# Kernel tuning notes

Hardware: AMD Instinct MI355X
Metric: run time of the kernel (lower is better)

## Reference

```python
import math
import jax, jax.numpy as jnp
import numpy as np

N_HEAD = 16
KNN = 4                     # config.knn_num
MEM_FRAC = 8.0              # config.mem_frac
INFLUENCE = 1.0             # config.knn_softmax_influence
RESID_FOUND = 0.5           # from set_resid_frac(resid_frac=0.5) (assumed split)
RESID_CURR = 0.5


def setup_inputs() -> dict:
    key = jax.random.key(0)
    ks = jax.random.split(key, 7)
    B, T, C, H, M = 1, 1024, 1024, N_HEAD, 8192
    d = C // H
    return {
        "x": jax.random.normal(ks[0], (B, T, C), jnp.float32),
        "c_attn_w": jax.random.normal(ks[1], (3 * C, C), jnp.float32) * 0.02,
        "c_attn_b": jax.random.normal(ks[2], (3 * C,), jnp.float32) * 0.01,
        "c_proj_w": jax.random.normal(ks[3], (C, C), jnp.float32) * 0.02,
        "c_proj_b": jax.random.normal(ks[4], (C,), jnp.float32) * 0.01,
        "key_store": jax.random.normal(ks[5], (H, M, d), jnp.float32),
        "value_store": jax.random.normal(ks[6], (H, M, d), jnp.float32),
    }


def _knn_get(att, k, q, v, key_store, value_store):
    # Faithful vectorized version of knn_get (batch must be 1, as in the
    # original whose scatter offsets i*t are only valid for b==1).
    B, H, T, d = k.shape
    scale = 1.0 / math.sqrt(d)
    # last-query attention row over all keys: (B,H,T)
    a = att[:, :, -1, :]
    # mem_frac thresholding (bookkeeping_frac falsy -> skipped)
    a = jnp.where(a < 1.0 / (MEM_FRAC * T), 0.0, a)
    sel = (a != 0.0)[0]                      # (H,T) selected positions
    kh, qh, vh = k[0], q[0], v[0]            # (H,T,d)
    # exact L2 search = faiss.IndexFlatL2: d2 = |k|^2 - 2 k.s + |s|^2
    d2 = (jnp.sum(kh * kh, -1, keepdims=True)
          - 2.0 * jnp.einsum('htd,hmd->htm', kh, key_store)
          + jnp.sum(key_store * key_store, -1)[:, None, :])   # (H,T,M)
    _, idx = jax.lax.top_k(-d2, KNN)         # (H,T,K) nearest neighbors
    idx = jnp.maximum(idx, 0)                # idx[idx<0]=0
    keys_f = jnp.take_along_axis(key_store[:, None, :, :], idx[..., None], axis=2)   # (H,T,K,d)
    vals_f = jnp.take_along_axis(value_store[:, None, :, :], idx[..., None], axis=2)
    # not resid_only: prepend current key/value -> stack size K+1
    keys_all = jnp.concatenate([kh[:, :, None, :], keys_f], axis=2)   # (H,T,S,d)
    vals_all = jnp.concatenate([vh[:, :, None, :], vals_f], axis=2)
    attf = jnp.einsum('htd,htsd->hts', qh, keys_all) * scale
    attf = jnp.where(jnp.isnan(attf), -jnp.inf, attf)
    w = jax.nn.softmax(attf * INFLUENCE, axis=-1)                     # softmax over the stack dim
    vals = jnp.einsum('hts,htsd->htd', w, vals_all)
    vals = vals * RESID_FOUND + vh * RESID_CURR                       # resid mix branch
    v_new = jnp.where(sel[..., None], vals, vh)                       # scatter back
    return v_new[None]                                                # (1,H,T,d)


def reference(x, c_attn_w, c_attn_b, c_proj_w, c_proj_b, key_store, value_store):
    B, T, C = x.shape
    H = key_store.shape[0]
    d = C // H
    qkv = x @ c_attn_w.T + c_attn_b
    q, k, v = jnp.split(qkv, 3, axis=2)
    heads = lambda t: t.reshape(B, T, H, d).transpose(0, 2, 1, 3)
    q, k, v = heads(q), heads(k), heads(v)
    logits = jnp.einsum('bhqd,bhkd->bhqk', q, k) * (1.0 / math.sqrt(d))
    causal = jnp.tril(jnp.ones((T, T), bool))
    logits = jnp.where(causal, logits, -jnp.inf)
    att = jax.nn.softmax(logits, axis=-1)
    # knn_get runs under torch.no_grad in the original
    v_new = jax.lax.stop_gradient(_knn_get(att, k, q, v, key_store, value_store))
    y = jnp.einsum('bhqk,bhkd->bhqd', att, v_new)   # dropout p=0 (eval)
    y = y.transpose(0, 2, 1, 3).reshape(B, T, C)
    return y @ c_proj_w.T + c_proj_b
```

## Files before the change

### kernel.cpp

```cpp
#include <hip/hip_runtime.h>
#include <math.h>

#define NH 16
#define TT 1024
#define CC 1024
#define DD 64
#define MM 8192
#define MQ 4
#define MQS (MM / MQ)

typedef __attribute__((ext_vector_type(8))) short short8;
typedef __attribute__((ext_vector_type(4))) float f32x4;

__device__ __forceinline__ float wredsum(float x) {
#pragma unroll
  for (int o = 32; o; o >>= 1) x += __shfl_xor(x, o);
  return x;
}
__device__ __forceinline__ unsigned int bf16rn(float x) {
  unsigned int u = __float_as_uint(x);
  return (u + 0x7fffu + ((u >> 16) & 1u)) >> 16;
}
__device__ __forceinline__ float bf16f(unsigned int h) {
  return __uint_as_float(h << 16);
}

__device__ __forceinline__ void ins4(float d, int i, float vd[4], int vi[4]) {
  if (d < vd[3] || (d == vd[3] && i < vi[3])) {
    vd[3] = d; vi[3] = i;
#pragma unroll
    for (int s = 3; s > 0; --s) {
      bool sw = (vd[s] < vd[s - 1]) || (vd[s] == vd[s - 1] && vi[s] < vi[s - 1]);
      if (sw) {
        float td = vd[s]; vd[s] = vd[s - 1]; vd[s - 1] = td;
        int ti = vi[s]; vi[s] = vi[s - 1]; vi[s - 1] = ti;
      }
    }
  }
}

__device__ __forceinline__ void stage_rows8_swz(const char* gRow0, size_t gStride, char* lds, int lane) {
  int rr = lane >> 3;
  int c = (lane & 7) ^ rr;
  __builtin_amdgcn_global_load_lds(
      (const __attribute__((address_space(1))) unsigned int*)(gRow0 + (size_t)rr * gStride + (c << 4)),
      (__attribute__((address_space(3))) unsigned int*)lds, 16, 0, 0);
}

__device__ __forceinline__ void conv_chunk(const float* __restrict__ src,
                                           char* __restrict__ hi, char* __restrict__ lo, int gc) {
  const float* p = src + ((size_t)gc << 3);
  float4 f0 = *(const float4*)p;
  float4 f1 = *(const float4*)(p + 4);
  float f[8] = {f0.x, f0.y, f0.z, f0.w, f1.x, f1.y, f1.z, f1.w};
  short8 hv, lv;
#pragma unroll
  for (int e = 0; e < 8; ++e) {
    unsigned hb = bf16rn(f[e]);
    hv[e] = (short)hb;
    lv[e] = (short)bf16rn(f[e] - bf16f(hb));
  }
  size_t off = (size_t)gc << 4;
  *(short8*)(hi + off) = hv;
  *(short8*)(lo + off) = lv;
}

__global__ void __launch_bounds__(256) convert_all(
    const float* __restrict__ x, char* __restrict__ xhi, char* __restrict__ xlo,
    const float* __restrict__ Wa, char* __restrict__ wahi, char* __restrict__ walo,
    const float* __restrict__ Wp, char* __restrict__ wphi, char* __restrict__ wplo,
    const float* __restrict__ ks, char* __restrict__ khi, char* __restrict__ klo,
    float* __restrict__ kn2)
{
  int b = blockIdx.x, tid = threadIdx.x;
  if (b < 512) { conv_chunk(x, xhi, xlo, b * 256 + tid); return; }
  if (b < 2048) { conv_chunk(Wa, wahi, walo, (b - 512) * 256 + tid); return; }
  if (b < 2560) { conv_chunk(Wp, wphi, wplo, (b - 2048) * 256 + tid); return; }
  int gc = (b - 2560) * 256 + tid;
  const float* p = ks + ((size_t)gc << 3);
  float4 f0 = *(const float4*)p;
  float4 f1 = *(const float4*)(p + 4);
  float f[8] = {f0.x, f0.y, f0.z, f0.w, f1.x, f1.y, f1.z, f1.w};
  float s = 0.f;
  short8 hv, lv;
#pragma unroll
  for (int e = 0; e < 8; ++e) {
    s = fmaf(f[e], f[e], s);
    unsigned hb = bf16rn(f[e]);
    hv[e] = (short)hb;
    lv[e] = (short)bf16rn(f[e] - bf16f(hb));
  }
  size_t off = (size_t)gc << 4;
  *(short8*)(khi + off) = hv;
  *(short8*)(klo + off) = lv;
  s += __shfl_xor(s, 1);
  s += __shfl_xor(s, 2);
  s += __shfl_xor(s, 4);
  if ((tid & 7) == 0) kn2[gc >> 3] = -0.5f * s;
}

__global__ void __launch_bounds__(256) gemm_qkv(
    const char* __restrict__ xhi, const char* __restrict__ xlo,
    const char* __restrict__ wahi, const char* __restrict__ walo,
    const float* __restrict__ ba, char* __restrict__ qhi, char* __restrict__ qlo)
{
  int n0 = blockIdx.x * 128, m0 = blockIdx.y * 64;
  int tid = threadIdx.x, lane = tid & 63, w = tid >> 6;
  int wr = w >> 1, wc = w & 1;
  int lr = lane & 15, lc = lane >> 4;
  __shared__ __align__(16) char smem[49152];
  char* sAhi = smem;
  char* sAlo = smem + 8192;
  char* sBhi = smem + 16384;
  char* sBlo = smem + 32768;
  f32x4 acc[2][4];
#pragma unroll
  for (int i = 0; i < 2; ++i)
#pragma unroll
    for (int j = 0; j < 4; ++j) acc[i][j] = (f32x4){0.f, 0.f, 0.f, 0.f};

  for (int kb = 0; kb < 16; ++kb) {
    if (kb) __syncthreads();
#pragma unroll
    for (int c8 = 0; c8 < 2; ++c8) {
      int r8 = w * 16 + c8 * 8;
      stage_rows8_swz(xhi + (size_t)(m0 + r8) * 2048 + (size_t)kb * 128, 2048, sAhi + r8 * 128, lane);
      stage_rows8_swz(xlo + (size_t)(m0 + r8) * 2048 + (size_t)kb * 128, 2048, sAlo + r8 * 128, lane);
    }
#pragma unroll
    for (int c8 = 0; c8 < 4; ++c8) {
      int r8 = w * 32 + c8 * 8;
      stage_rows8_swz(wahi + (size_t)(n0 + r8) * 2048 + (size_t)kb * 128, 2048, sBhi + r8 * 128, lane);
      stage_rows8_swz(walo + (size_t)(n0 + r8) * 2048 + (size_t)kb * 128, 2048, sBlo + r8 * 128, lane);
    }
    __syncthreads();
#pragma unroll
    for (int kh = 0; kh < 2; ++kh) {
      short8 ah[2], al[2], bh[4], bl[4];
#pragma unroll
      for (int mi = 0; mi < 2; ++mi) {
        int ra = wr * 32 + mi * 16 + lr;
        int ca = ((kh * 4 + lc) ^ (ra & 7)) << 4;
        ah[mi] = *(const short8*)(sAhi + ra * 128 + ca);
        al[mi] = *(const short8*)(sAlo + ra * 128 + ca);
      }
#pragma unroll
      for (int nj = 0; nj < 4; ++nj) {
        int rb = wc * 64 + nj * 16 + lr;
        int cb = ((kh * 4 + lc) ^ (rb & 7)) << 4;
        bh[nj] = *(const short8*)(sBhi + rb * 128 + cb);
        bl[nj] = *(const short8*)(sBlo + rb * 128 + cb);
      }
#pragma unroll
      for (int mi = 0; mi < 2; ++mi)
#pragma unroll
        for (int nj = 0; nj < 4; ++nj) {
          acc[mi][nj] = __builtin_amdgcn_mfma_f32_16x16x32_bf16(ah[mi], bh[nj], acc[mi][nj], 0, 0, 0);
          acc[mi][nj] = __builtin_amdgcn_mfma_f32_16x16x32_bf16(al[mi], bh[nj], acc[mi][nj], 0, 0, 0);
          acc[mi][nj] = __builtin_amdgcn_mfma_f32_16x16x32_bf16(ah[mi], bl[nj], acc[mi][nj], 0, 0, 0);
        }
    }
  }

  __syncthreads();
  char* hbuf = smem + w * 9216;
  char* lbuf = hbuf + 4608;
#pragma unroll
  for (int mi = 0; mi < 2; ++mi)
#pragma unroll
    for (int nj = 0; nj < 4; ++nj)
#pragma unroll
      for (int r = 0; r < 4; ++r) {
        int row = mi * 16 + lc * 4 + r;
        int col = nj * 16 + lr;
        float v = acc[mi][nj][r] + ba[n0 + wc * 64 + col];
        unsigned hb = bf16rn(v);
        *(unsigned short*)(hbuf + row * 144 + col * 2) = (unsigned short)hb;
        *(unsigned short*)(lbuf + row * 144 + col * 2) = (unsigned short)bf16rn(v - bf16f(hb));
      }
#pragma unroll
  for (int ps = 0; ps < 4; ++ps) {
    int rr = ps * 8 + (lane >> 3);
    int c = lane & 7;
    size_t gb = ((size_t)(m0 + wr * 32 + rr) * 3072 + n0 + wc * 64) * 2 + (c << 4);
    *(uint4*)(qhi + gb) = *(const uint4*)(hbuf + rr * 144 + c * 16);
    *(uint4*)(qlo + gb) = *(const uint4*)(lbuf + rr * 144 + c * 16);
  }
}

#define QSLDS 2304
__global__ void __launch_bounds__(512) qk_softmax(
    const char* __restrict__ qhi, const char* __restrict__ qlo,
    char* __restrict__ attB, float* __restrict__ attlast)
{
  int rb = blockIdx.x, h = blockIdx.y;
  int i0 = rb * 32;
  int tid = threadIdx.x, lane = tid & 63, w = tid >> 6;
  int wr = w >> 2, wcg = w & 3;
  int lr = lane & 15, lc = lane >> 4;
  __shared__ float redm[2][16][4];
  __shared__ float reds[2][16][4];
  __shared__ __align__(16) char tb[8][2 * QSLDS];

  int iq = i0 + wr * 16 + lr;
  short8 ah[2], al[2];
  {
    size_t qb = (size_t)iq * 6144 + h * 128;
#pragma unroll
    for (int kh = 0; kh < 2; ++kh) {
      size_t off = qb + ((kh * 4 + lc) << 4);
      ah[kh] = *(const short8*)(qhi + off);
      al[kh] = *(const short8*)(qlo + off);
    }
  }

  f32x4 acc[16];
#pragma unroll
  for (int nt = 0; nt < 16; ++nt) acc[nt] = (f32x4){0.f, 0.f, 0.f, 0.f};

  int maxj = i0 + 31;
#pragma unroll
  for (int nt = 0; nt < 16; ++nt) {
    if (wcg * 256 + nt * 16 <= maxj) {
      int jr = wcg * 256 + nt * 16 + lr;
      size_t kb = (size_t)jr * 6144 + 2048 + h * 128;
      short8 bh[2], bl[2];
#pragma unroll
      for (int kh = 0; kh < 2; ++kh) {
        size_t off = kb + ((kh * 4 + lc) << 4);
        bh[kh] = *(const short8*)(qhi + off);
        bl[kh] = *(const short8*)(qlo + off);
      }
#pragma unroll
      for (int kh = 0; kh < 2; ++kh) {
        acc[nt] = __builtin_amdgcn_mfma_f32_16x16x32_bf16(ah[kh], bh[kh], acc[nt], 0, 0, 0);
        acc[nt] = __builtin_amdgcn_mfma_f32_16x16x32_bf16(al[kh], bh[kh], acc[nt], 0, 0, 0);
        acc[nt] = __builtin_amdgcn_mfma_f32_16x16x32_bf16(ah[kh], bl[kh], acc[nt], 0, 0, 0);
      }
    }
  }

  int iv[4];
  float pmax[4];
#pragma unroll
  for (int r = 0; r < 4; ++r) {
    iv[r] = i0 + wr * 16 + lc * 4 + r;
    pmax[r] = -INFINITY;
  }
#pragma unroll
  for (int nt = 0; nt < 16; ++nt) {
    int j = wcg * 256 + nt * 16 + lr;
#pragma unroll
    for (int r = 0; r < 4; ++r) {
      float v = (j <= iv[r]) ? acc[nt][r] * 0.125f : -INFINITY;
      acc[nt][r] = v;
      pmax[r] = fmaxf(pmax[r], v);
    }
  }
#pragma unroll
  for (int o = 1; o <= 8; o <<= 1)
#pragma unroll
    for (int r = 0; r < 4; ++r) pmax[r] = fmaxf(pmax[r], __shfl_xor(pmax[r], o));
  if (lr == 0) {
#pragma unroll
    for (int r = 0; r < 4; ++r) redm[wr][lc * 4 + r][wcg] = pmax[r];
  }
  __syncthreads();
  float rowm[4];
#pragma unroll
  for (int r = 0; r < 4; ++r) {
    float* q = redm[wr][lc * 4 + r];
    rowm[r] = fmaxf(fmaxf(q[0], q[1]), fmaxf(q[2], q[3]));
  }

  float psum[4] = {0.f, 0.f, 0.f, 0.f};
#pragma unroll
  for (int nt = 0; nt < 16; ++nt)
#pragma unroll
    for (int r = 0; r < 4; ++r) {
      float e = __expf(acc[nt][r] - rowm[r]);
      acc[nt][r] = e;
      psum[r] += e;
    }
#pragma unroll
  for (int o = 1; o <= 8; o <<= 1)
#pragma unroll
    for (int r = 0; r < 4; ++r) psum[r] += __shfl_xor(psum[r], o);
  if (lr == 0) {
#pragma unroll
    for (int r = 0; r < 4; ++r) reds[wr][lc * 4 + r][wcg] = psum[r];
  }
  __syncthreads();
  float inv[4];
#pragma unroll
  for (int r = 0; r < 4; ++r) {
    float* q = reds[wr][lc * 4 + r];
    inv[r] = 1.0f / (q[0] + q[1] + q[2] + q[3]);
  }

  char* mybuf = tb[w];
  int iv0 = i0 + wr * 16;
#pragma unroll
  for (int cc = 0; cc < 4; ++cc) {
#pragma unroll
    for (int q = 0; q < 4; ++q) {
      int nt = cc * 4 + q;
      int col = q * 16 + lr;
#pragma unroll
      for (int r = 0; r < 4; ++r) {
        int row = lc * 4 + r;
        float v = acc[nt][r] * inv[r];
        unsigned hb = bf16rn(v);
        unsigned lb = bf16rn(v - bf16f(hb));
        *(unsigned short*)(mybuf + row * 144 + col * 2) = (unsigned short)hb;
        *(unsigned short*)(mybuf + QSLDS + row * 144 + col * 2) = (unsigned short)lb;
        if (iv[r] == 1023) attlast[(h << 10) + wcg * 256 + cc * 64 + col] = v;
      }
    }
    __syncthreads();
#pragma unroll
    for (int half = 0; half < 2; ++half) {
      int rr = (lane >> 3) + half * 8;
      int c = lane & 7;
      int rowg = iv0 + rr;
      uint4 hv = *(const uint4*)(mybuf + rr * 144 + c * 16);
      uint4 lv = *(const uint4*)(mybuf + QSLDS + rr * 144 + c * 16);
      size_t basep = ((size_t)h << 22) + ((size_t)rowg << 12)
                   + (size_t)(((wcg << 2) + cc) << 7) + (size_t)(c << 4);
      *(uint4*)(attB + basep) = hv;
      *(uint4*)(attB + basep + 2048) = lv;
    }
    __syncthreads();
  }
}

#define BUFB 16384

#define TOPK_STEP(PAR, DO_STAGE)                                              \
  {                                                                           \
    if (DO_STAGE) {                                                           \
      _Pragma("unroll")                                                       \
      for (int i2 = 0; i2 < 4; ++i2) {                                        \
        __builtin_amdgcn_global_load_lds(                                     \
            (const __attribute__((address_space(1))) unsigned int*)stsrc[i2], \
            (__attribute__((address_space(3))) unsigned int*)(stdst[i2] + ((PAR) ^ 16384)), \
            16, 0, 0);                                                        \
        stsrc[i2] += 8192;                                                    \
      }                                                                       \
    }                                                                         \
    f32x4 acc[4];                                                             \
    _Pragma("unroll")                                                         \
    for (int ms = 0; ms < 4; ++ms)                                            \
      acc[ms] = *(const f32x4*)(knp + ms * 64);                               \
    knp += 256;                                                               \
    _Pragma("unroll")                                                         \
    for (int ms = 0; ms < 4; ++ms) {                                          \
      short8 ah0 = *(const short8*)(frg[ms * 2 + 0] + (PAR));                 \
      short8 al0 = *(const short8*)(frg[ms * 2 + 0] + (PAR) + 8192);          \
      short8 ah1 = *(const short8*)(frg[ms * 2 + 1] + (PAR));                 \
      short8 al1 = *(const short8*)(frg[ms * 2 + 1] + (PAR) + 8192);          \
      acc[ms] = __builtin_amdgcn_mfma_f32_16x16x32_bf16(ah0, bhi[0], acc[ms], 0, 0, 0); \
      acc[ms] = __builtin_amdgcn_mfma_f32_16x16x32_bf16(al0, bhi[0], acc[ms], 0, 0, 0); \
      acc[ms] = __builtin_amdgcn_mfma_f32_16x16x32_bf16(ah0, blo[0], acc[ms], 0, 0, 0); \
      acc[ms] = __builtin_amdgcn_mfma_f32_16x16x32_bf16(ah1, bhi[1], acc[ms], 0, 0, 0); \
      acc[ms] = __builtin_amdgcn_mfma_f32_16x16x32_bf16(al1, bhi[1], acc[ms], 0, 0, 0); \
      acc[ms] = __builtin_amdgcn_mfma_f32_16x16x32_bf16(ah1, blo[1], acc[ms], 0, 0, 0); \
    }                                                                         \
    float pk[16];                                                             \
    _Pragma("unroll")                                                         \
    for (int ms = 0; ms < 4; ++ms)                                            \
      _Pragma("unroll")                                                       \
      for (int r = 0; r < 4; ++r) {                                           \
        unsigned u = __float_as_uint(acc[ms][r]);                             \
        pk[ms * 4 + r] = __uint_as_float((u & ~15u) | (unsigned)(ms * 4 + r)); \
      }                                                                       \
    float mx = pk[0];                                                         \
    _Pragma("unroll")                                                         \
    for (int c = 1; c < 16; ++c) mx = fmaxf(mx, pk[c]);                       \
    while (mx > ba[3]) {                                                      \
      unsigned pb = __float_as_uint(mx);                                      \
      int cl = pb & 15;                                                       \
      ba[3] = mx; bi_[3] = mg0 + ((cl & 12) << 2) + (cl & 3);                 \
      _Pragma("unroll")                                                       \
      for (int s = 3; s > 0; --s)                                             \
        if (ba[s] > ba[s - 1]) {                                              \
          float td = ba[s]; ba[s] = ba[s - 1]; ba[s - 1] = td;                \
          int ti = bi_[s]; bi_[s] = bi_[s - 1]; bi_[s - 1] = ti;              \
        }                                                                     \
      _Pragma("unroll")                                                       \
      for (int c2 = 0; c2 < 16; ++c2)                                         \
        if (pk[c2] == mx) pk[c2] = -3.0e38f;                                  \
      mx = pk[0];                                                             \
      _Pragma("unroll")                                                       \
      for (int c2 = 1; c2 < 16; ++c2) mx = fmaxf(mx, pk[c2]);                 \
    }                                                                         \
    mg0 += 64;                                                                \
    __syncthreads();                                                          \
  }

__global__ void __launch_bounds__(256, 4) topk_mfma(
    const char* __restrict__ qhi, const char* __restrict__ qlo,
    const char* __restrict__ khi, const char* __restrict__ klo,
    const float* __restrict__ kn2, float* __restrict__ pd, int* __restrict__ pi)
{
  int bid = blockIdx.x;
  int h = bid & 15, ttile = (bid >> 4) & 15, mq = bid >> 8;
  int tid = threadIdx.x, lane = tid & 63, w = tid >> 6;
  int t0 = ttile * 64 + w * 16;
  __shared__ __align__(16) char smem[2 * BUFB];

  short8 bhi[2], blo[2];
  {
    int t = t0 + (lane & 15);
    size_t rb = (size_t)t * 6144 + 2048 + h * 128;
#pragma unroll
    for (int kh = 0; kh < 2; ++kh) {
      size_t off = rb + ((kh * 4 + (lane >> 4)) << 4);
      bhi[kh] = *(const short8*)(qhi + off);
      blo[kh] = *(const short8*)(qlo + off);
    }
  }

  const char* ghi = khi + ((size_t)h * MM + (size_t)mq * MQS) * 128;
  const char* glo = klo + ((size_t)h * MM + (size_t)mq * MQS) * 128;
  const char* knp = (const char*)(kn2 + (size_t)h * MM + (size_t)mq * MQS + ((lane >> 4) << 2));

  float ba[4] = {-3.0e38f, -3.0e38f, -3.0e38f, -3.0e38f};
  int   bi_[4] = {-1, -1, -1, -1};

  const char* stsrc[4];
  char* stdst[4];
  {
    int rr = lane >> 3;
    size_t laneoff = (size_t)rr * 128 + (((lane & 7) ^ rr) << 4);
#pragma unroll
    for (int i2 = 0; i2 < 4; ++i2) {
      int s = w * 4 + i2;
      stsrc[i2] = ((s < 8) ? (ghi + s * 1024) : (glo + (s - 8) * 1024)) + laneoff;
      stdst[i2] = smem + s * 1024;
    }
  }
  char* frg[8];
#pragma unroll
  for (int ms = 0; ms < 4; ++ms)
#pragma unroll
    for (int kh = 0; kh < 2; ++kh) {
      int mloc = ms * 16 + (lane & 15);
      int c = kh * 4 + (lane >> 4);
      frg[ms * 2 + kh] = smem + mloc * 128 + ((c ^ (mloc & 7)) << 4);
    }

#pragma unroll
  for (int i2 = 0; i2 < 4; ++i2) {
    __builtin_amdgcn_global_load_lds(
        (const __attribute__((address_space(1))) unsigned int*)stsrc[i2],
        (__attribute__((address_space(3))) unsigned int*)stdst[i2], 16, 0, 0);
    stsrc[i2] += 8192;
  }
  __syncthreads();

  int mg0 = mq * MQS + ((lane >> 4) << 2);
  for (int it2 = 0; it2 < 16; ++it2) {
    TOPK_STEP(0, true)
    TOPK_STEP(16384, (it2 < 15))
  }

  float bd[4];
#pragma unroll
  for (int s = 0; s < 4; ++s) bd[s] = ba[s] * -2.0f;
#pragma unroll
  for (int st = 16; st <= 32; st <<= 1) {
    float sd[4]; int si[4];
#pragma unroll
    for (int s = 0; s < 4; ++s) {
      sd[s] = __shfl_xor(bd[s], st);
      si[s] = __shfl_xor(bi_[s], st);
    }
#pragma unroll
    for (int s = 0; s < 4; ++s) ins4(sd[s], si[s], bd, bi_);
  }
  if (lane < 16) {
    size_t o = (((size_t)mq * NH + h) * TT + (t0 + lane)) * 4;
#pragma unroll
    for (int s = 0; s < 4; ++s) { pd[o + s] = bd[s]; pi[o + s] = bi_[s]; }
  }
}

__global__ void __launch_bounds__(1024) knn_attend(
    const char* __restrict__ qhi, const char* __restrict__ qlo,
    const float* __restrict__ attlast,
    const float* __restrict__ pd, const int* __restrict__ pi,
    const float* __restrict__ kstore, const float* __restrict__ vstore,
    char* __restrict__ vThi, char* __restrict__ vTlo)
{
  __shared__ __align__(16) unsigned short hiT[64][72];
  __shared__ __align__(16) unsigned short loT[64][72];
  int tid = threadIdx.x, lane = tid & 63, w = tid >> 6;
  int h = blockIdx.x >> 4, t0 = (blockIdx.x & 15) << 6;

#pragma unroll
  for (int i = 0; i < 4; ++i) {
    int t = t0 + w * 4 + i;
    int g = (h << 10) + t;

    float fd[4]; int fi[4];
    {
      size_t o = ((size_t)(lane & 3) * (NH * TT) + g) * 4;
#pragma unroll
      for (int s = 0; s < 4; ++s) { fd[s] = pd[o + s]; fi[s] = pi[o + s]; }
#pragma unroll
      for (int st = 1; st <= 2; st <<= 1) {
        float sd[4]; int si[4];
#pragma unroll
        for (int s = 0; s < 4; ++s) {
          sd[s] = __shfl_xor(fd[s], st);
          si[s] = __shfl_xor(fi[s], st);
        }
#pragma unroll
        for (int s = 0; s < 4; ++s) ins4(sd[s], si[s], fd, fi);
      }
    }

    size_t rb = (size_t)t * 6144 + h * 128 + lane * 2;
    float q = bf16f(*(const unsigned short*)(qhi + rb)) + bf16f(*(const unsigned short*)(qlo + rb));
    float k = bf16f(*(const unsigned short*)(qhi + rb + 2048)) + bf16f(*(const unsigned short*)(qlo + rb + 2048));
    float v = bf16f(*(const unsigned short*)(qhi + rb + 4096)) + bf16f(*(const unsigned short*)(qlo + rb + 4096));
    float al = attlast[g];
    bool sel = al >= (1.0f / 8192.0f);

    float attf[5], vf[5];
    attf[0] = wredsum(q * k) * 0.125f;
    vf[0] = v;
#pragma unroll
    for (int s = 1; s < 5; ++s) {
      int m = fi[s - 1];
      const float* kp = kstore + ((size_t)h * MM + m) * DD;
      const float* vp = vstore + ((size_t)h * MM + m) * DD;
      attf[s] = wredsum(q * kp[lane]) * 0.125f;
      vf[s] = vp[lane];
    }
    float mx = attf[0];
#pragma unroll
    for (int s = 1; s < 5; ++s) mx = fmaxf(mx, attf[s]);
    float wgt[5], sum = 0.f;
#pragma unroll
    for (int s = 0; s < 5; ++s) { wgt[s] = __expf(attf[s] - mx); sum += wgt[s]; }
    float inv = 1.0f / sum;
    float vals = 0.f;
#pragma unroll
    for (int s = 0; s < 5; ++s) vals = fmaf(wgt[s] * inv, vf[s], vals);
    float r = 0.5f * vals + 0.5f * v;
    float vn = sel ? r : v;

    unsigned hb = bf16rn(vn);
    hiT[lane][t - t0] = (unsigned short)hb;
    loT[lane][t - t0] = (unsigned short)bf16rn(vn - bf16f(hb));
  }
  __syncthreads();

  int half = tid >> 9;
  int idx = tid & 511;
  int r = idx >> 3, c = idx & 7;
  const unsigned short* src = half ? &loT[r][c * 8] : &hiT[r][c * 8];
  uint4 vv = *(const uint4*)src;
  char* dst = (half ? vTlo : vThi) + (size_t)((h << 6) + r) * 2048 + ((size_t)t0 << 1) + (c << 4);
  *(uint4*)dst = vv;
}

__global__ void __launch_bounds__(256) gemm_attv(
    const char* __restrict__ attB, const char* __restrict__ vThi, const char* __restrict__ vTlo,
    char* __restrict__ Yhi, char* __restrict__ Ylo)
{
  int h = blockIdx.y, m0 = blockIdx.x * 128;
  const char* aBase = attB + (size_t)h * 4194304;
  int tid = threadIdx.x, lane = tid & 63, w = tid >> 6;
  int wr = w >> 1, wc = w & 1;
  __shared__ __align__(16) char smem[49152];
  char* sAhi = smem;
  char* sAlo = smem + 16384;
  char* sBhi = smem + 32768;
  char* sBlo = smem + 40960;
  f32x4 acc[4][2];
#pragma unroll
  for (int i = 0; i < 4; ++i)
#pragma unroll
    for (int j = 0; j < 2; ++j) acc[i][j] = (f32x4){0.f, 0.f, 0.f, 0.f};
  int lr = lane & 15, lc = lane >> 4;
  int kbEnd = ((m0 + 127) >> 6) + 1;
  if (kbEnd > 16) kbEnd = 16;
  for (int kb = 0; kb < kbEnd; ++kb) {
    if (kb) __syncthreads();
#pragma unroll
    for (int c8 = 0; c8 < 4; ++c8) {
      int r8 = w * 32 + c8 * 8;
      stage_rows8_swz(aBase + (size_t)(m0 + r8) * 4096 + (size_t)kb * 128, 4096, sAhi + r8 * 128, lane);
      stage_rows8_swz(aBase + (size_t)(m0 + r8) * 4096 + 2048 + (size_t)kb * 128, 4096, sAlo + r8 * 128, lane);
    }
#pragma unroll
    for (int c8 = 0; c8 < 2; ++c8) {
      int r8 = w * 16 + c8 * 8;
      stage_rows8_swz(vThi + (size_t)((h << 6) + r8) * 2048 + (size_t)kb * 128, 2048, sBhi + r8 * 128, lane);
      stage_rows8_swz(vTlo + (size_t)((h << 6) + r8) * 2048 + (size_t)kb * 128, 2048, sBlo + r8 * 128, lane);
    }
    __syncthreads();
#pragma unroll
    for (int kh = 0; kh < 2; ++kh) {
      short8 ah[4], al[4], bh[2], bl[2];
#pragma unroll
      for (int f = 0; f < 4; ++f) {
        int ra = wr * 64 + f * 16 + lr;
        int ca = ((kh * 4 + lc) ^ (ra & 7)) << 4;
        ah[f] = *(const short8*)(sAhi + ra * 128 + ca);
        al[f] = *(const short8*)(sAlo + ra * 128 + ca);
      }
#pragma unroll
      for (int f = 0; f < 2; ++f) {
        int rbr = wc * 32 + f * 16 + lr;
        int cb = ((kh * 4 + lc) ^ (rbr & 7)) << 4;
        bh[f] = *(const short8*)(sBhi + rbr * 128 + cb);
        bl[f] = *(const short8*)(sBlo + rbr * 128 + cb);
      }
#pragma unroll
      for (int mi = 0; mi < 4; ++mi)
#pragma unroll
        for (int nj = 0; nj < 2; ++nj) {
          acc[mi][nj] = __builtin_amdgcn_mfma_f32_16x16x32_bf16(ah[mi], bh[nj], acc[mi][nj], 0, 0, 0);
          acc[mi][nj] = __builtin_amdgcn_mfma_f32_16x16x32_bf16(al[mi], bh[nj], acc[mi][nj], 0, 0, 0);
          acc[mi][nj] = __builtin_amdgcn_mfma_f32_16x16x32_bf16(ah[mi], bl[nj], acc[mi][nj], 0, 0, 0);
        }
    }
  }
#pragma unroll
  for (int mi = 0; mi < 4; ++mi)
#pragma unroll
    for (int nj = 0; nj < 2; ++nj)
#pragma unroll
      for (int r = 0; r < 4; ++r) {
        int m = m0 + wr * 64 + mi * 16 + lc * 4 + r;
        int n = (h << 6) + wc * 32 + nj * 16 + lr;
        float v = acc[mi][nj][r];
        unsigned hb = bf16rn(v);
        size_t off = ((size_t)m * 1024 + n) * 2;
        *(unsigned short*)(Yhi + off) = (unsigned short)hb;
        *(unsigned short*)(Ylo + off) = (unsigned short)bf16rn(v - bf16f(hb));
      }
}

__global__ void __launch_bounds__(256) gemm_out(
    const char* __restrict__ yhi, const char* __restrict__ ylo,
    const char* __restrict__ wphi, const char* __restrict__ wplo,
    const float* __restrict__ bp, float* __restrict__ out)
{
  int n0 = blockIdx.x * 64, m0 = blockIdx.y * 64;
  int tid = threadIdx.x, lane = tid & 63, w = tid >> 6;
  int wr = w >> 1, wc = w & 1;
  int lr = lane & 15, lc = lane >> 4;
  __shared__ __align__(16) char smem[32768];
  char* sAhi = smem;
  char* sAlo = smem + 8192;
  char* sBhi = smem + 16384;
  char* sBlo = smem + 24576;
  f32x4 acc[2][2];
#pragma unroll
  for (int i = 0; i < 2; ++i)
#pragma unroll
    for (int j = 0; j < 2; ++j) acc[i][j] = (f32x4){0.f, 0.f, 0.f, 0.f};

  for (int kb = 0; kb < 16; ++kb) {
    if (kb) __syncthreads();
#pragma unroll
    for (int c8 = 0; c8 < 2; ++c8) {
      int r8 = w * 16 + c8 * 8;
      stage_rows8_swz(yhi + (size_t)(m0 + r8) * 2048 + (size_t)kb * 128, 2048, sAhi + r8 * 128, lane);
      stage_rows8_swz(ylo + (size_t)(m0 + r8) * 2048 + (size_t)kb * 128, 2048, sAlo + r8 * 128, lane);
      stage_rows8_swz(wphi + (size_t)(n0 + r8) * 2048 + (size_t)kb * 128, 2048, sBhi + r8 * 128, lane);
      stage_rows8_swz(wplo + (size_t)(n0 + r8) * 2048 + (size_t)kb * 128, 2048, sBlo + r8 * 128, lane);
    }
    __syncthreads();
#pragma unroll
    for (int kh = 0; kh < 2; ++kh) {
      short8 ah[2], al[2], bh[2], bl[2];
#pragma unroll
      for (int mi = 0; mi < 2; ++mi) {
        int ra = wr * 32 + mi * 16 + lr;
        int ca = ((kh * 4 + lc) ^ (ra & 7)) << 4;
        ah[mi] = *(const short8*)(sAhi + ra * 128 + ca);
        al[mi] = *(const short8*)(sAlo + ra * 128 + ca);
      }
#pragma unroll
      for (int nj = 0; nj < 2; ++nj) {
        int rb = wc * 32 + nj * 16 + lr;
        int cb = ((kh * 4 + lc) ^ (rb & 7)) << 4;
        bh[nj] = *(const short8*)(sBhi + rb * 128 + cb);
        bl[nj] = *(const short8*)(sBlo + rb * 128 + cb);
      }
#pragma unroll
      for (int mi = 0; mi < 2; ++mi)
#pragma unroll
        for (int nj = 0; nj < 2; ++nj) {
          acc[mi][nj] = __builtin_amdgcn_mfma_f32_16x16x32_bf16(ah[mi], bh[nj], acc[mi][nj], 0, 0, 0);
          acc[mi][nj] = __builtin_amdgcn_mfma_f32_16x16x32_bf16(al[mi], bh[nj], acc[mi][nj], 0, 0, 0);
          acc[mi][nj] = __builtin_amdgcn_mfma_f32_16x16x32_bf16(ah[mi], bl[nj], acc[mi][nj], 0, 0, 0);
        }
    }
  }
#pragma unroll
  for (int mi = 0; mi < 2; ++mi)
#pragma unroll
    for (int nj = 0; nj < 2; ++nj)
#pragma unroll
      for (int r = 0; r < 4; ++r) {
        int m = m0 + wr * 32 + mi * 16 + lc * 4 + r;
        int n = n0 + wc * 32 + nj * 16 + lr;
        out[(size_t)m * 1024 + n] = acc[mi][nj][r] + bp[n];
      }
}

extern "C" void kernel_launch(void* const* d_in, const int* in_sizes, int n_in,
                              void* d_out, int out_size, void* d_ws, size_t ws_size,
                              hipStream_t stream) {
  (void)in_sizes; (void)n_in; (void)out_size; (void)ws_size;
  const float* x  = (const float*)d_in[0];
  const float* Wa = (const float*)d_in[1];
  const float* ba = (const float*)d_in[2];
  const float* Wp = (const float*)d_in[3];
  const float* bp = (const float*)d_in[4];
  const float* Ks = (const float*)d_in[5];
  const float* Vs = (const float*)d_in[6];
  float* out = (float*)d_out;

  char* base = (char*)d_ws;
  char* xhi  = base;
  char* xlo  = base + 0x200000;
  char* wahi = base + 0x400000;
  char* walo = base + 0xA00000;
  char* khi  = base + 0x1000000;
  char* klo  = base + 0x2000000;
  char*  attB = base;
  char* tail = base + 0x4000000;
  char* qhi = tail;
  char* qlo = tail + 0x600000;
  float* attlast = (float*)(tail + 0xC00000);
  float* kn2     = (float*)(tail + 0xC10000);
  float* pd      = (float*)(tail + 0xC90000);
  int*   pi      = (int*)(tail + 0xE90000);
  char* vThi = tail + 0x1090000;
  char* vTlo = tail + 0x1290000;
  char* yhi  = tail + 0x1490000;
  char* ylo  = tail + 0x1690000;
  char* wphi = tail + 0x1890000;
  char* wplo = tail + 0x1A90000;

  hipLaunchKernelGGL(convert_all, dim3(6656), dim3(256), 0, stream,
                     x, xhi, xlo, Wa, wahi, walo, Wp, wphi, wplo, Ks, khi, klo, kn2);
  hipLaunchKernelGGL(gemm_qkv, dim3(24, 16), dim3(256), 0, stream,
                     (const char*)xhi, (const char*)xlo, (const char*)wahi, (const char*)walo,
                     ba, qhi, qlo);
  hipLaunchKernelGGL(topk_mfma, dim3(16 * 16 * MQ), dim3(256), 0, stream,
                     (const char*)qhi, (const char*)qlo, (const char*)khi, (const char*)klo,
                     kn2, pd, pi);
  hipLaunchKernelGGL(qk_softmax, dim3(32, 16), dim3(512), 0, stream,
                     (const char*)qhi, (const char*)qlo, attB, attlast);
  hipLaunchKernelGGL(knn_attend, dim3(256), dim3(1024), 0, stream,
                     (const char*)qhi, (const char*)qlo, attlast, pd, pi, Ks, Vs, vThi, vTlo);
  hipLaunchKernelGGL(gemm_attv, dim3(8, 16), dim3(256), 0, stream,
                     (const char*)attB, (const char*)vThi, (const char*)vTlo, yhi, ylo);
  hipLaunchKernelGGL(gemm_out, dim3(16, 16), dim3(256), 0, stream,
                     (const char*)yhi, (const char*)ylo, (const char*)wphi, (const char*)wplo,
                     bp, out);
}
```

Baseline: 217.0 us.

## Fuse QK softmax with PV product, compute last attention row separately

```diff
diff --git a/kernel.cpp b/kernel.cpp
--- a/kernel.cpp
+++ b/kernel.cpp
@@ -188,150 +188,47 @@
   }
 }
 
-#define QSLDS 2304
-__global__ void __launch_bounds__(512) qk_softmax(
-    const char* __restrict__ qhi, const char* __restrict__ qlo,
-    char* __restrict__ attB, float* __restrict__ attlast)
+__global__ void __launch_bounds__(1024) attlast_k(
+    const char* __restrict__ qhi, const char* __restrict__ qlo, float* __restrict__ attlast)
 {
-  int rb = blockIdx.x, h = blockIdx.y;
-  int i0 = rb * 32;
-  int tid = threadIdx.x, lane = tid & 63, w = tid >> 6;
-  int wr = w >> 2, wcg = w & 3;
-  int lr = lane & 15, lc = lane >> 4;
-  __shared__ float redm[2][16][4];
-  __shared__ float reds[2][16][4];
-  __shared__ __align__(16) char tb[8][2 * QSLDS];
-
-  int iq = i0 + wr * 16 + lr;
-  short8 ah[2], al[2];
-  {
-    size_t qb = (size_t)iq * 6144 + h * 128;
-#pragma unroll
-    for (int kh = 0; kh < 2; ++kh) {
-      size_t off = qb + ((kh * 4 + lc) << 4);
-      ah[kh] = *(const short8*)(qhi + off);
-      al[kh] = *(const short8*)(qlo + off);
-    }
-  }
-
-  f32x4 acc[16];
-#pragma unroll
-  for (int nt = 0; nt < 16; ++nt) acc[nt] = (f32x4){0.f, 0.f, 0.f, 0.f};
-
-  int maxj = i0 + 31;
-#pragma unroll
-  for (int nt = 0; nt < 16; ++nt) {
-    if (wcg * 256 + nt * 16 <= maxj) {
-      int jr = wcg * 256 + nt * 16 + lr;
-      size_t kb = (size_t)jr * 6144 + 2048 + h * 128;
-      short8 bh[2], bl[2];
-#pragma unroll
-      for (int kh = 0; kh < 2; ++kh) {
-        size_t off = kb + ((kh * 4 + lc) << 4);
-        bh[kh] = *(const short8*)(qhi + off);
-        bl[kh] = *(const short8*)(qlo + off);
-      }
-#pragma unroll
-      for (int kh = 0; kh < 2; ++kh) {
-        acc[nt] = __builtin_amdgcn_mfma_f32_16x16x32_bf16(ah[kh], bh[kh], acc[nt], 0, 0, 0);
-        acc[nt] = __builtin_amdgcn_mfma_f32_16x16x32_bf16(al[kh], bh[kh], acc[nt], 0, 0, 0);
-        acc[nt] = __builtin_amdgcn_mfma_f32_16x16x32_bf16(ah[kh], bl[kh], acc[nt], 0, 0, 0);
-      }
-    }
-  }
-
-  int iv[4];
-  float pmax[4];
-#pragma unroll
-  for (int r = 0; r < 4; ++r) {
-    iv[r] = i0 + wr * 16 + lc * 4 + r;
-    pmax[r] = -INFINITY;
-  }
-#pragma unroll
-  for (int nt = 0; nt < 16; ++nt) {
-    int j = wcg * 256 + nt * 16 + lr;
-#pragma unroll
-    for (int r = 0; r < 4; ++r) {
-      float v = (j <= iv[r]) ? acc[nt][r] * 0.125f : -INFINITY;
-      acc[nt][r] = v;
-      pmax[r] = fmaxf(pmax[r], v);
-    }
-  }
-#pragma unroll
-  for (int o = 1; o <= 8; o <<= 1)
-#pragma unroll
-    for (int r = 0; r < 4; ++r) pmax[r] = fmaxf(pmax[r], __shfl_xor(pmax[r], o));
-  if (lr == 0) {
-#pragma unroll
-    for (int r = 0; r < 4; ++r) redm[wr][lc * 4 + r][wcg] = pmax[r];
-  }
-  __syncthreads();
-  float rowm[4];
-#pragma unroll
-  for (int r = 0; r < 4; ++r) {
-    float* q = redm[wr][lc * 4 + r];
-    rowm[r] = fmaxf(fmaxf(q[0], q[1]), fmaxf(q[2], q[3]));
-  }
-
-  float psum[4] = {0.f, 0.f, 0.f, 0.f};
-#pragma unroll
-  for (int nt = 0; nt < 16; ++nt)
-#pragma unroll
-    for (int r = 0; r < 4; ++r) {
-      float e = __expf(acc[nt][r] - rowm[r]);
-      acc[nt][r] = e;
-      psum[r] += e;
-    }
-#pragma unroll
-  for (int o = 1; o <= 8; o <<= 1)
-#pragma unroll
-    for (int r = 0; r < 4; ++r) psum[r] += __shfl_xor(psum[r], o);
-  if (lr == 0) {
-#pragma unroll
-    for (int r = 0; r < 4; ++r) reds[wr][lc * 4 + r][wcg] = psum[r];
-  }
-  __syncthreads();
-  float inv[4];
-#pragma unroll
-  for (int r = 0; r < 4; ++r) {
-    float* q = reds[wr][lc * 4 + r];
-    inv[r] = 1.0f / (q[0] + q[1] + q[2] + q[3]);
-  }
-
-  char* mybuf = tb[w];
-  int iv0 = i0 + wr * 16;
-#pragma unroll
-  for (int cc = 0; cc < 4; ++cc) {
-#pragma unroll
-    for (int q = 0; q < 4; ++q) {
-      int nt = cc * 4 + q;
-      int col = q * 16 + lr;
-#pragma unroll
-      for (int r = 0; r < 4; ++r) {
-        int row = lc * 4 + r;
-        float v = acc[nt][r] * inv[r];
-        unsigned hb = bf16rn(v);
-        unsigned lb = bf16rn(v - bf16f(hb));
-        *(unsigned short*)(mybuf + row * 144 + col * 2) = (unsigned short)hb;
-        *(unsigned short*)(mybuf + QSLDS + row * 144 + col * 2) = (unsigned short)lb;
-        if (iv[r] == 1023) attlast[(h << 10) + wcg * 256 + cc * 64 + col] = v;
-      }
-    }
-    __syncthreads();
-#pragma unroll
-    for (int half = 0; half < 2; ++half) {
-      int rr = (lane >> 3) + half * 8;
-      int c = lane & 7;
-      int rowg = iv0 + rr;
-      uint4 hv = *(const uint4*)(mybuf + rr * 144 + c * 16);
-      uint4 lv = *(const uint4*)(mybuf + QSLDS + rr * 144 + c * 16);
-      size_t basep = ((size_t)h << 22) + ((size_t)rowg << 12)
-                   + (size_t)(((wcg << 2) + cc) << 7) + (size_t)(c << 4);
-      *(uint4*)(attB + basep) = hv;
-      *(uint4*)(attB + basep + 2048) = lv;
-    }
-    __syncthreads();
-  }
+  int h = blockIdx.x;
+  int j = threadIdx.x, lane = j & 63, wv = j >> 6;
+  __shared__ float qrow[64];
+  __shared__ float redmx[16], redsm[16];
+  if (j < 64) {
+    size_t qb = (size_t)1023 * 6144 + h * 128 + j * 2;
+    qrow[j] = bf16f(*(const unsigned short*)(qhi + qb)) + bf16f(*(const unsigned short*)(qlo + qb));
+  }
+  __syncthreads();
+  size_t kb = (size_t)j * 6144 + 2048 + (size_t)h * 128;
+  float s = 0.f;
+#pragma unroll
+  for (int c8 = 0; c8 < 8; ++c8) {
+    short8 khv = *(const short8*)(qhi + kb + c8 * 16);
+    short8 klv = *(const short8*)(qlo + kb + c8 * 16);
+#pragma unroll
+    for (int e = 0; e < 8; ++e) {
+      float kv = bf16f((unsigned short)khv[e]) + bf16f((unsigned short)klv[e]);
+      s = fmaf(kv, qrow[c8 * 8 + e], s);
+    }
+  }
+  s *= 0.125f;
+  float m = s;
+#pragma unroll
+  for (int o = 32; o; o >>= 1) m = fmaxf(m, __shfl_xor(m, o));
+  if (lane == 0) redmx[wv] = m;
+  __syncthreads();
+  float M = redmx[0];
+#pragma unroll
+  for (int q = 1; q < 16; ++q) M = fmaxf(M, redmx[q]);
+  float e = __expf(s - M);
+  float ws = wredsum(e);
+  if (lane == 0) redsm[wv] = ws;
+  __syncthreads();
+  float S = redsm[0];
+#pragma unroll
+  for (int q = 1; q < 16; ++q) S += redsm[q];
+  attlast[(h << 10) + j] = e / S;
 }
 
 #define BUFB 16384
@@ -567,83 +464,189 @@
   *(uint4*)dst = vv;
 }
 
-__global__ void __launch_bounds__(256) gemm_attv(
-    const char* __restrict__ attB, const char* __restrict__ vThi, const char* __restrict__ vTlo,
+#define QSLDS 2304
+__global__ void __launch_bounds__(512) qk_softmax_pv(
+    const char* __restrict__ qhi, const char* __restrict__ qlo,
+    const char* __restrict__ vThi, const char* __restrict__ vTlo,
     char* __restrict__ Yhi, char* __restrict__ Ylo)
 {
-  int h = blockIdx.y, m0 = blockIdx.x * 128;
-  const char* aBase = attB + (size_t)h * 4194304;
+  int rb = blockIdx.x, h = blockIdx.y;
+  int i0 = rb * 32;
   int tid = threadIdx.x, lane = tid & 63, w = tid >> 6;
-  int wr = w >> 1, wc = w & 1;
-  __shared__ __align__(16) char smem[49152];
-  char* sAhi = smem;
-  char* sAlo = smem + 16384;
-  char* sBhi = smem + 32768;
-  char* sBlo = smem + 40960;
-  f32x4 acc[4][2];
-#pragma unroll
-  for (int i = 0; i < 4; ++i)
-#pragma unroll
-    for (int j = 0; j < 2; ++j) acc[i][j] = (f32x4){0.f, 0.f, 0.f, 0.f};
+  int wr = w >> 2, wcg = w & 3;
   int lr = lane & 15, lc = lane >> 4;
-  int kbEnd = ((m0 + 127) >> 6) + 1;
-  if (kbEnd > 16) kbEnd = 16;
-  for (int kb = 0; kb < kbEnd; ++kb) {
-    if (kb) __syncthreads();
-#pragma unroll
-    for (int c8 = 0; c8 < 4; ++c8) {
-      int r8 = w * 32 + c8 * 8;
-      stage_rows8_swz(aBase + (size_t)(m0 + r8) * 4096 + (size_t)kb * 128, 4096, sAhi + r8 * 128, lane);
-      stage_rows8_swz(aBase + (size_t)(m0 + r8) * 4096 + 2048 + (size_t)kb * 128, 4096, sAlo + r8 * 128, lane);
-    }
-#pragma unroll
-    for (int c8 = 0; c8 < 2; ++c8) {
-      int r8 = w * 16 + c8 * 8;
-      stage_rows8_swz(vThi + (size_t)((h << 6) + r8) * 2048 + (size_t)kb * 128, 2048, sBhi + r8 * 128, lane);
-      stage_rows8_swz(vTlo + (size_t)((h << 6) + r8) * 2048 + (size_t)kb * 128, 2048, sBlo + r8 * 128, lane);
-    }
-    __syncthreads();
+  __shared__ float redm[2][16][4];
+  __shared__ float reds[2][16][4];
+  __shared__ __align__(16) char tb[8][2 * QSLDS];
+
+  int iq = i0 + wr * 16 + lr;
+  short8 ah[2], al[2];
+  {
+    size_t qb = (size_t)iq * 6144 + h * 128;
 #pragma unroll
     for (int kh = 0; kh < 2; ++kh) {
-      short8 ah[4], al[4], bh[2], bl[2];
-#pragma unroll
-      for (int f = 0; f < 4; ++f) {
-        int ra = wr * 64 + f * 16 + lr;
-        int ca = ((kh * 4 + lc) ^ (ra & 7)) << 4;
-        ah[f] = *(const short8*)(sAhi + ra * 128 + ca);
-        al[f] = *(const short8*)(sAlo + ra * 128 + ca);
-      }
-#pragma unroll
-      for (int f = 0; f < 2; ++f) {
-        int rbr = wc * 32 + f * 16 + lr;
-        int cb = ((kh * 4 + lc) ^ (rbr & 7)) << 4;
-        bh[f] = *(const short8*)(sBhi + rbr * 128 + cb);
-        bl[f] = *(const short8*)(sBlo + rbr * 128 + cb);
-      }
-#pragma unroll
-      for (int mi = 0; mi < 4; ++mi)
-#pragma unroll
-        for (int nj = 0; nj < 2; ++nj) {
-          acc[mi][nj] = __builtin_amdgcn_mfma_f32_16x16x32_bf16(ah[mi], bh[nj], acc[mi][nj], 0, 0, 0);
-          acc[mi][nj] = __builtin_amdgcn_mfma_f32_16x16x32_bf16(al[mi], bh[nj], acc[mi][nj], 0, 0, 0);
-          acc[mi][nj] = __builtin_amdgcn_mfma_f32_16x16x32_bf16(ah[mi], bl[nj], acc[mi][nj], 0, 0, 0);
+      size_t off = qb + ((kh * 4 + lc) << 4);
+      ah[kh] = *(const short8*)(qhi + off);
+      al[kh] = *(const short8*)(qlo + off);
+    }
+  }
+
+  f32x4 acc[16];
+#pragma unroll
+  for (int nt = 0; nt < 16; ++nt) acc[nt] = (f32x4){0.f, 0.f, 0.f, 0.f};
+
+  int maxj = i0 + 31;
+#pragma unroll
+  for (int nt = 0; nt < 16; ++nt) {
+    if (wcg * 256 + nt * 16 <= maxj) {
+      int jr = wcg * 256 + nt * 16 + lr;
+      size_t kb = (size_t)jr * 6144 + 2048 + h * 128;
+      short8 bh[2], bl[2];
+#pragma unroll
+      for (int kh = 0; kh < 2; ++kh) {
+        size_t off = kb + ((kh * 4 + lc) << 4);
+        bh[kh] = *(const short8*)(qhi + off);
+        bl[kh] = *(const short8*)(qlo + off);
+      }
+#pragma unroll
+      for (int kh = 0; kh < 2; ++kh) {
+        acc[nt] = __builtin_amdgcn_mfma_f32_16x16x32_bf16(ah[kh], bh[kh], acc[nt], 0, 0, 0);
+        acc[nt] = __builtin_amdgcn_mfma_f32_16x16x32_bf16(al[kh], bh[kh], acc[nt], 0, 0, 0);
+        acc[nt] = __builtin_amdgcn_mfma_f32_16x16x32_bf16(ah[kh], bl[kh], acc[nt], 0, 0, 0);
+      }
+    }
+  }
+
+  int iv[4];
+  float pmax[4];
+#pragma unroll
+  for (int r = 0; r < 4; ++r) {
+    iv[r] = i0 + wr * 16 + lc * 4 + r;
+    pmax[r] = -INFINITY;
+  }
+#pragma unroll
+  for (int nt = 0; nt < 16; ++nt) {
+    int j = wcg * 256 + nt * 16 + lr;
+#pragma unroll
+    for (int r = 0; r < 4; ++r) {
+      float v = (j <= iv[r]) ? acc[nt][r] * 0.125f : -INFINITY;
+      acc[nt][r] = v;
+      pmax[r] = fmaxf(pmax[r], v);
+    }
+  }
+#pragma unroll
+  for (int o = 1; o <= 8; o <<= 1)
+#pragma unroll
+    for (int r = 0; r < 4; ++r) pmax[r] = fmaxf(pmax[r], __shfl_xor(pmax[r], o));
+  if (lr == 0) {
+#pragma unroll
+    for (int r = 0; r < 4; ++r) redm[wr][lc * 4 + r][wcg] = pmax[r];
+  }
+  __syncthreads();
+  float rowm[4];
+#pragma unroll
+  for (int r = 0; r < 4; ++r) {
+    float* q = redm[wr][lc * 4 + r];
+    rowm[r] = fmaxf(fmaxf(q[0], q[1]), fmaxf(q[2], q[3]));
+  }
+
+  float psum[4] = {0.f, 0.f, 0.f, 0.f};
+#pragma unroll
+  for (int nt = 0; nt < 16; ++nt)
+#pragma unroll
+    for (int r = 0; r < 4; ++r) {
+      float e = __expf(acc[nt][r] - rowm[r]);
+      acc[nt][r] = e;
+      psum[r] += e;
+    }
+#pragma unroll
+  for (int o = 1; o <= 8; o <<= 1)
+#pragma unroll
+    for (int r = 0; r < 4; ++r) psum[r] += __shfl_xor(psum[r], o);
+  if (lr == 0) {
+#pragma unroll
+    for (int r = 0; r < 4; ++r) reds[wr][lc * 4 + r][wcg] = psum[r];
+  }
+  __syncthreads();
+  float inv[4];
+#pragma unroll
+  for (int r = 0; r < 4; ++r) {
+    float* q = reds[wr][lc * 4 + r];
+    inv[r] = 1.0f / (q[0] + q[1] + q[2] + q[3]);
+  }
+
+  char* mybuf = tb[w];
+  f32x4 accy[4];
+#pragma unroll
+  for (int ct = 0; ct < 4; ++ct) accy[ct] = (f32x4){0.f, 0.f, 0.f, 0.f};
+#pragma unroll
+  for (int cc = 0; cc < 4; ++cc) {
+    int j0 = wcg * 256 + cc * 64;
+    if (j0 <= maxj) {
+#pragma unroll
+      for (int q = 0; q < 4; ++q) {
+        int nt = cc * 4 + q;
+        int col = q * 16 + lr;
+#pragma unroll
+        for (int r = 0; r < 4; ++r) {
+          int row = lc * 4 + r;
+          float v = acc[nt][r] * inv[r];
+          unsigned hb = bf16rn(v);
+          *(unsigned short*)(mybuf + row * 144 + col * 2) = (unsigned short)hb;
+          *(unsigned short*)(mybuf + QSLDS + row * 144 + col * 2) = (unsigned short)bf16rn(v - bf16f(hb));
         }
-    }
-  }
-#pragma unroll
-  for (int mi = 0; mi < 4; ++mi)
-#pragma unroll
-    for (int nj = 0; nj < 2; ++nj)
-#pragma unroll
-      for (int r = 0; r < 4; ++r) {
-        int m = m0 + wr * 64 + mi * 16 + lc * 4 + r;
-        int n = (h << 6) + wc * 32 + nj * 16 + lr;
-        float v = acc[mi][nj][r];
-        unsigned hb = bf16rn(v);
-        size_t off = ((size_t)m * 1024 + n) * 2;
-        *(unsigned short*)(Yhi + off) = (unsigned short)hb;
-        *(unsigned short*)(Ylo + off) = (unsigned short)bf16rn(v - bf16f(hb));
-      }
+      }
+#pragma unroll
+      for (int kh2 = 0; kh2 < 2; ++kh2) {
+        const char* abase = mybuf + lr * 144 + kh2 * 64 + lc * 16;
+        short8 pa_h = *(const short8*)(abase);
+        short8 pa_l = *(const short8*)(abase + QSLDS);
+        size_t vb = (size_t)(h << 6) * 2048 + (size_t)(j0 + kh2 * 32 + lc * 8) * 2;
+#pragma unroll
+        for (int ct = 0; ct < 4; ++ct) {
+          size_t vroff = (size_t)(ct * 16 + lr) * 2048;
+          short8 vb_h = *(const short8*)(vThi + vb + vroff);
+          short8 vb_l = *(const short8*)(vTlo + vb + vroff);
+          accy[ct] = __builtin_amdgcn_mfma_f32_16x16x32_bf16(pa_h, vb_h, accy[ct], 0, 0, 0);
+          accy[ct] = __builtin_amdgcn_mfma_f32_16x16x32_bf16(pa_l, vb_h, accy[ct], 0, 0, 0);
+          accy[ct] = __builtin_amdgcn_mfma_f32_16x16x32_bf16(pa_h, vb_l, accy[ct], 0, 0, 0);
+        }
+      }
+    }
+  }
+
+  float* yp = (float*)mybuf;
+#pragma unroll
+  for (int ct = 0; ct < 4; ++ct)
+#pragma unroll
+    for (int r = 0; r < 4; ++r)
+      yp[(lc * 4 + r) * 64 + ct * 16 + lr] = accy[ct][r];
+  __syncthreads();
+
+  int row32 = tid >> 4;
+  int c4 = (tid & 15) * 4;
+  int wrr = row32 >> 4;
+  float vsum[4];
+#pragma unroll
+  for (int e = 0; e < 4; ++e) {
+    float s = 0.f;
+#pragma unroll
+    for (int g = 0; g < 4; ++g)
+      s += ((const float*)(tb[wrr * 4 + g]))[(row32 & 15) * 64 + c4 + e];
+    vsum[e] = s;
+  }
+  unsigned hs[4], ls[4];
+#pragma unroll
+  for (int e = 0; e < 4; ++e) {
+    hs[e] = bf16rn(vsum[e]);
+    ls[e] = bf16rn(vsum[e] - bf16f(hs[e]));
+  }
+  size_t off = ((size_t)(i0 + row32) * 1024 + (h << 6) + c4) * 2;
+  uint2 hv2, lv2;
+  hv2.x = hs[0] | (hs[1] << 16); hv2.y = hs[2] | (hs[3] << 16);
+  lv2.x = ls[0] | (ls[1] << 16); lv2.y = ls[2] | (ls[3] << 16);
+  *(uint2*)(Yhi + off) = hv2;
+  *(uint2*)(Ylo + off) = lv2;
 }
 
 __global__ void __launch_bounds__(256) gemm_out(
@@ -736,7 +739,6 @@
   char* walo = base + 0xA00000;
   char* khi  = base + 0x1000000;
   char* klo  = base + 0x2000000;
-  char*  attB = base;
   char* tail = base + 0x4000000;
   char* qhi = tail;
   char* qlo = tail + 0x600000;
@@ -759,12 +761,13 @@
   hipLaunchKernelGGL(topk_mfma, dim3(16 * 16 * MQ), dim3(256), 0, stream,
                      (const char*)qhi, (const char*)qlo, (const char*)khi, (const char*)klo,
                      kn2, pd, pi);
-  hipLaunchKernelGGL(qk_softmax, dim3(32, 16), dim3(512), 0, stream,
-                     (const char*)qhi, (const char*)qlo, attB, attlast);
+  hipLaunchKernelGGL(attlast_k, dim3(NH), dim3(1024), 0, stream,
+                     (const char*)qhi, (const char*)qlo, attlast);
   hipLaunchKernelGGL(knn_attend, dim3(256), dim3(1024), 0, stream,
                      (const char*)qhi, (const char*)qlo, attlast, pd, pi, Ks, Vs, vThi, vTlo);
-  hipLaunchKernelGGL(gemm_attv, dim3(8, 16), dim3(256), 0, stream,
-                     (const char*)attB, (const char*)vThi, (const char*)vTlo, yhi, ylo);
+  hipLaunchKernelGGL(qk_softmax_pv, dim3(32, 16), dim3(512), 0, stream,
+                     (const char*)qhi, (const char*)qlo, (const char*)vThi, (const char*)vTlo,
+                     yhi, ylo);
   hipLaunchKernelGGL(gemm_out, dim3(16, 16), dim3(256), 0, stream,
                      (const char*)yhi, (const char*)ylo, (const char*)wphi, (const char*)wplo,
                      bp, out);
```

After: 229.8 us. 1.06x slower.
